# Optimization experiments

Measured on AMD Instinct MI355X. Metric: run time of the kernel, lower is better.

The kernel has to match this reference:

```python
import jax, jax.numpy as jnp
import numpy as np

B, N, K = 16, 4096, 128

def setup_inputs() -> dict:
    key = jax.random.key(0)
    k1, k2, k3, k4, k5 = jax.random.split(key, 5)
    positions = jax.random.normal(k1, (B, N, 3), dtype=jnp.float32) * 5.0
    neighbors = jax.random.randint(k2, (B, N, K), 0, N, dtype=jnp.int32)
    neighbor_mask = (jax.random.uniform(k3, (B, N, K)) < 0.9).astype(jnp.float32)
    cell = jax.random.normal(k4, (B, 3, 3), dtype=jnp.float32) + 10.0 * jnp.eye(3, dtype=jnp.float32)
    cell_offsets = jax.random.randint(k5, (B, N, K, 3), -1, 2).astype(jnp.float32)
    return {
        "positions": positions,
        "neighbors": neighbors,
        "neighbor_mask": neighbor_mask,
        "cell": cell,
        "cell_offsets": cell_offsets,
    }

def reference(positions, neighbors, neighbor_mask, cell, cell_offsets):
    # Gather neighbor positions: [B,N,K,3]
    pos_j = jax.vmap(lambda p, n: p[n])(positions, neighbors)
    # Relative vectors r_j - r_i
    dist_vec = pos_j - positions[:, :, None, :]
    # Periodic boundary correction: offsets @ cell, [B,N,K,3]
    dist_vec = dist_vec + jnp.einsum("bnkd,bde->bnke", cell_offsets, cell)
    sq = jnp.sum(dist_vec * dist_vec, axis=-1)  # [B,N,K]
    mask = neighbor_mask > 0
    # Masked distances (safe sqrt: avoid sqrt(0) grad issues on masked entries)
    distances = jnp.where(mask, jnp.sqrt(jnp.where(mask, sq, 1.0)), 0.0)
    return distances
```

## Files before the change

### kernel.cpp

```cpp
#include <hip/hip_runtime.h>
#include <math.h>

constexpr int B = 16;
constexpr int N = 4096;
constexpr int K = 128;

constexpr int ROWS_PER_BLOCK = 128;
constexpr int THREADS = 512;
constexpr int EPC     = THREADS * 4;
constexpr int CHUNKS  = (ROWS_PER_BLOCK * K) / EPC;
constexpr int SLOTS   = 4;
constexpr int AHEAD   = 3;

typedef float fx4 __attribute__((ext_vector_type(4)));
typedef int   ix4 __attribute__((ext_vector_type(4)));


struct Chunk {
    ix4 jj;
    fx4 mm, o0, o1, o2;
};

__device__ __forceinline__ void load_chunk(Chunk& c,
                                           const int*   __restrict__ nbr,
                                           const float* __restrict__ mask,
                                           const float* __restrict__ offs,
                                           size_t e0) {
    c.jj = __builtin_nontemporal_load((const ix4*)(nbr  + e0));
    c.mm = __builtin_nontemporal_load((const fx4*)(mask + e0));
    const fx4* __restrict__ p = (const fx4*)(offs + e0 * 3);
    c.o0 = p[0];
    c.o1 = p[1];
    c.o2 = p[2];
}

__global__ __launch_bounds__(THREADS, 4)
void pairwise_dist_deep(const float* __restrict__ pos,
                        const int*   __restrict__ nbr,
                        const float* __restrict__ mask,
                        const float* __restrict__ cell,
                        const float* __restrict__ offs,
                        float*       __restrict__ out) {
    __shared__ fx4 spos[N];

    const int tid   = threadIdx.x;
    const int b     = blockIdx.x >> 5;
    const int rblk  = blockIdx.x & 31;
    const int nbase = rblk * ROWS_PER_BLOCK;

    {
        const fx4* __restrict__ pb4 = (const fx4*)(pos + (size_t)b * N * 3);
        const fx4 r0 = pb4[tid * 6 + 0];
        const fx4 r1 = pb4[tid * 6 + 1];
        const fx4 r2 = pb4[tid * 6 + 2];
        const fx4 r3 = pb4[tid * 6 + 3];
        const fx4 r4 = pb4[tid * 6 + 4];
        const fx4 r5 = pb4[tid * 6 + 5];
        const int a0 = tid * 8;
        spos[a0 + 0] = (fx4){r0.x, r0.y, r0.z, 0.f};
        spos[a0 + 1] = (fx4){r0.w, r1.x, r1.y, 0.f};
        spos[a0 + 2] = (fx4){r1.z, r1.w, r2.x, 0.f};
        spos[a0 + 3] = (fx4){r2.y, r2.z, r2.w, 0.f};
        spos[a0 + 4] = (fx4){r3.x, r3.y, r3.z, 0.f};
        spos[a0 + 5] = (fx4){r3.w, r4.x, r4.y, 0.f};
        spos[a0 + 6] = (fx4){r4.z, r4.w, r5.x, 0.f};
        spos[a0 + 7] = (fx4){r5.y, r5.z, r5.w, 0.f};
    }

    const float* __restrict__ cb = cell + b * 9;
    const float c00 = cb[0], c01 = cb[1], c02 = cb[2];
    const float c10 = cb[3], c11 = cb[4], c12 = cb[5];
    const float c20 = cb[6], c21 = cb[7], c22 = cb[8];

    const size_t blockElemBase = ((size_t)b * N + nbase) * K;

    Chunk win[SLOTS];
#pragma unroll
    for (int c = 0; c < AHEAD; ++c)
        load_chunk(win[c], nbr, mask, offs,
                   blockElemBase + (size_t)c * EPC + (size_t)tid * 4);
    __builtin_amdgcn_sched_barrier(0);

    __syncthreads();

#pragma unroll
    for (int c = 0; c < CHUNKS; ++c) {
        if (c + AHEAD < CHUNKS) {
            load_chunk(win[(c + AHEAD) % SLOTS], nbr, mask, offs,
                       blockElemBase + (size_t)(c + AHEAD) * EPC +
                       (size_t)tid * 4);
            __builtin_amdgcn_sched_barrier(0);
        }

        const Chunk& cur = win[c % SLOTS];

        const int    eLocal = c * EPC + tid * 4;
        const size_t e0     = blockElemBase + eLocal;
        const int    n      = nbase + (eLocal >> 7);
        const fx4    pi     = spos[n];

        const float ox[4] = {cur.o0.x, cur.o0.w, cur.o1.z, cur.o2.y};
        const float oy[4] = {cur.o0.y, cur.o1.x, cur.o1.w, cur.o2.z};
        const float oz[4] = {cur.o0.z, cur.o1.y, cur.o2.x, cur.o2.w};
        const int   j [4] = {cur.jj.x, cur.jj.y, cur.jj.z, cur.jj.w};
        const float m [4] = {cur.mm.x, cur.mm.y, cur.mm.z, cur.mm.w};

        float res[4];
#pragma unroll
        for (int i = 0; i < 4; ++i) {
            const fx4 pj = spos[j[i]];
            const float dx = (pj.x - pi.x) + ox[i] * c00 + oy[i] * c10 + oz[i] * c20;
            const float dy = (pj.y - pi.y) + ox[i] * c01 + oy[i] * c11 + oz[i] * c21;
            const float dz = (pj.z - pi.z) + ox[i] * c02 + oy[i] * c12 + oz[i] * c22;
            const float sq = dx * dx + dy * dy + dz * dz;
            res[i] = (m[i] > 0.0f) ? __builtin_amdgcn_sqrtf(sq) : 0.0f;
        }

        const fx4 r = {res[0], res[1], res[2], res[3]};
        __builtin_nontemporal_store(r, (fx4*)(out + e0));
    }
}

extern "C" void kernel_launch(void* const* d_in, const int* in_sizes, int n_in,
                              void* d_out, int out_size, void* d_ws, size_t ws_size,
                              hipStream_t stream) {
    const float* positions     = (const float*)d_in[0];
    const int*   neighbors     = (const int*)  d_in[1];
    const float* neighbor_mask = (const float*)d_in[2];
    const float* cell          = (const float*)d_in[3];
    const float* cell_offsets  = (const float*)d_in[4];
    float*       out           = (float*)d_out;

    const int blocks = B * (N / ROWS_PER_BLOCK);

    pairwise_dist_deep<<<blocks, THREADS, 0, stream>>>(
        positions, neighbors, neighbor_mask, cell, cell_offsets, out);
}
```

Measured before the change: 209.2 us.

## Stage streamed inputs through LDS with direct global-to-LDS async loads

```diff
diff --git a/kernel.cpp b/kernel.cpp
--- a/kernel.cpp
+++ b/kernel.cpp
@@ -7,46 +7,121 @@
 
 constexpr int ROWS_PER_BLOCK = 128;
 constexpr int THREADS = 512;
+constexpr int WAVES   = THREADS / 64;
 constexpr int EPC     = THREADS * 4;
 constexpr int CHUNKS  = (ROWS_PER_BLOCK * K) / EPC;
-constexpr int SLOTS   = 4;
-constexpr int AHEAD   = 3;
+constexpr int DEPTH   = 2;
+
+constexpr int SLAB_B  = 5 * 1024;
+
 
 typedef float fx4 __attribute__((ext_vector_type(4)));
 typedef int   ix4 __attribute__((ext_vector_type(4)));
 
+#define AS1(p) ((const __attribute__((address_space(1))) void*)(p))
+#define AS3(p) ((__attribute__((address_space(3))) void*)(p))
 
-struct Chunk {
-    ix4 jj;
-    fx4 mm, o0, o1, o2;
+struct Ctx {
+    const int*   nbr;
+    const float* mask;
+    const float* offs;
+    float*       out;
+    size_t base;
+    int    nbase, wv, lane;
+    float  c00, c01, c02, c10, c11, c12, c20, c21, c22;
 };
 
-__device__ __forceinline__ void load_chunk(Chunk& c,
-                                           const int*   __restrict__ nbr,
-                                           const float* __restrict__ mask,
-                                           const float* __restrict__ offs,
-                                           size_t e0) {
-    c.jj = __builtin_nontemporal_load((const ix4*)(nbr  + e0));
-    c.mm = __builtin_nontemporal_load((const fx4*)(mask + e0));
-    const fx4* __restrict__ p = (const fx4*)(offs + e0 * 3);
-    c.o0 = p[0];
-    c.o1 = p[1];
-    c.o2 = p[2];
+template<int CC>
+__device__ __forceinline__ void stage_chunk(const Ctx& x, char* slabs) {
+    constexpr int slot = CC & (DEPTH - 1);
+    char* slab = slabs + slot * (WAVES * SLAB_B);
+    const size_t slice = x.base + (size_t)CC * EPC + (size_t)x.wv * 256;
+    const int*   gn = x.nbr  + slice     + x.lane * 4;
+    const float* gm = x.mask + slice     + x.lane * 4;
+    const float* go = x.offs + slice * 3 + x.lane * 4;
+    __builtin_amdgcn_global_load_lds(AS1(gn),       AS3(slab),        16, 0, 0);
+    __builtin_amdgcn_global_load_lds(AS1(gm),       AS3(slab + 1024), 16, 0, 0);
+    __builtin_amdgcn_global_load_lds(AS1(go),       AS3(slab + 2048), 16, 0, 0);
+    __builtin_amdgcn_global_load_lds(AS1(go + 256), AS3(slab + 3072), 16, 0, 0);
+    __builtin_amdgcn_global_load_lds(AS1(go + 512), AS3(slab + 4096), 16, 0, 0);
+    __builtin_amdgcn_sched_barrier(0);
 }
 
-__global__ __launch_bounds__(THREADS, 4)
-void pairwise_dist_deep(const float* __restrict__ pos,
-                        const int*   __restrict__ nbr,
-                        const float* __restrict__ mask,
-                        const float* __restrict__ cell,
-                        const float* __restrict__ offs,
-                        float*       __restrict__ out) {
+template<int C>
+__device__ __forceinline__ void chunk_body(const Ctx& x, const fx4* spos,
+                                           char* slabs) {
+    constexpr int slot = C & (DEPTH - 1);
+    constexpr int NW = (C == 0) ? 5 : ((C == CHUNKS - 1) ? 1 : 6);
+    asm volatile("s_waitcnt vmcnt(%0)" :: "n"(NW) : "memory");
+    __builtin_amdgcn_sched_barrier(0);
+
+    const char* slab = slabs + slot * (WAVES * SLAB_B);
+    const ix4 jj = *(const ix4*)(slab + x.lane * 16);
+    const fx4 mm = *(const fx4*)(slab + 1024 + x.lane * 16);
+    const char* ob = slab + 2048 + x.lane * 48;
+    const fx4 o0 = *(const fx4*)(ob);
+    const fx4 o1 = *(const fx4*)(ob + 16);
+    const fx4 o2 = *(const fx4*)(ob + 32);
+
+    const int n  = x.nbase + C * (EPC / K) + x.wv * 2 + (x.lane >> 5);
+    const fx4 pi = spos[n];
+
+    const float ox[4] = {o0.x, o0.w, o1.z, o2.y};
+    const float oy[4] = {o0.y, o1.x, o1.w, o2.z};
+    const float oz[4] = {o0.z, o1.y, o2.x, o2.w};
+    const int   j [4] = {jj.x, jj.y, jj.z, jj.w};
+    const float m [4] = {mm.x, mm.y, mm.z, mm.w};
+
+    float res[4];
+#pragma unroll
+    for (int i = 0; i < 4; ++i) {
+        const fx4 pj = spos[j[i]];
+        const float dx = (pj.x - pi.x) + ox[i]*x.c00 + oy[i]*x.c10 + oz[i]*x.c20;
+        const float dy = (pj.y - pi.y) + ox[i]*x.c01 + oy[i]*x.c11 + oz[i]*x.c21;
+        const float dz = (pj.z - pi.z) + ox[i]*x.c02 + oy[i]*x.c12 + oz[i]*x.c22;
+        const float sq = dx*dx + dy*dy + dz*dz;
+        res[i] = (m[i] > 0.0f) ? __builtin_amdgcn_sqrtf(sq) : 0.0f;
+    }
+    const fx4 r = {res[0], res[1], res[2], res[3]};
+    const size_t e0 = x.base + (size_t)C * EPC + (size_t)x.wv * 256
+                      + (size_t)x.lane * 4;
+    __builtin_nontemporal_store(r, (fx4*)(x.out + e0));
+
+    if constexpr (C + DEPTH < CHUNKS) {
+        asm volatile("s_waitcnt lgkmcnt(0)" ::: "memory");
+        __builtin_amdgcn_sched_barrier(0);
+        stage_chunk<C + DEPTH>(x, slabs);
+    }
+}
+
+template<int C>
+__device__ __forceinline__ void run_chunks(const Ctx& x, const fx4* spos,
+                                           char* slabs) {
+    chunk_body<C>(x, spos, slabs);
+    if constexpr (C + 1 < CHUNKS) run_chunks<C + 1>(x, spos, slabs);
+}
+
+__global__ __launch_bounds__(THREADS)
+void pairwise_dist_dma(const float* __restrict__ pos,
+                       const int*   __restrict__ nbr,
+                       const float* __restrict__ mask,
+                       const float* __restrict__ cell,
+                       const float* __restrict__ offs,
+                       float*       __restrict__ out) {
     __shared__ fx4 spos[N];
+    __shared__ fx4 stagebuf[DEPTH][WAVES][SLAB_B / 16];
 
     const int tid   = threadIdx.x;
+    const int wv    = tid >> 6;
+    const int lane  = tid & 63;
     const int b     = blockIdx.x >> 5;
     const int rblk  = blockIdx.x & 31;
     const int nbase = rblk * ROWS_PER_BLOCK;
+
+    const float* __restrict__ cb = cell + b * 9;
+    const float c00 = cb[0], c01 = cb[1], c02 = cb[2];
+    const float c10 = cb[3], c11 = cb[4], c12 = cb[5];
+    const float c20 = cb[6], c21 = cb[7], c22 = cb[8];
 
     {
         const fx4* __restrict__ pb4 = (const fx4*)(pos + (size_t)b * N * 3);
@@ -67,58 +142,24 @@
         spos[a0 + 7] = (fx4){r5.y, r5.z, r5.w, 0.f};
     }
 
-    const float* __restrict__ cb = cell + b * 9;
-    const float c00 = cb[0], c01 = cb[1], c02 = cb[2];
-    const float c10 = cb[3], c11 = cb[4], c12 = cb[5];
-    const float c20 = cb[6], c21 = cb[7], c22 = cb[8];
+    Ctx x;
+    x.nbr = nbr; x.mask = mask; x.offs = offs; x.out = out;
+    x.base  = ((size_t)b * N + nbase) * K;
+    x.nbase = nbase; x.wv = wv; x.lane = lane;
+    x.c00 = c00; x.c01 = c01; x.c02 = c02;
+    x.c10 = c10; x.c11 = c11; x.c12 = c12;
+    x.c20 = c20; x.c21 = c21; x.c22 = c22;
 
-    const size_t blockElemBase = ((size_t)b * N + nbase) * K;
+    char* slabs = (char*)&stagebuf[0][wv][0];
 
-    Chunk win[SLOTS];
-#pragma unroll
-    for (int c = 0; c < AHEAD; ++c)
-        load_chunk(win[c], nbr, mask, offs,
-                   blockElemBase + (size_t)c * EPC + (size_t)tid * 4);
+    stage_chunk<0>(x, slabs);
+    stage_chunk<1>(x, slabs);
+
+    asm volatile("s_waitcnt lgkmcnt(0)" ::: "memory");
+    __builtin_amdgcn_s_barrier();
     __builtin_amdgcn_sched_barrier(0);
 
-    __syncthreads();
-
-#pragma unroll
-    for (int c = 0; c < CHUNKS; ++c) {
-        if (c + AHEAD < CHUNKS) {
-            load_chunk(win[(c + AHEAD) % SLOTS], nbr, mask, offs,
-                       blockElemBase + (size_t)(c + AHEAD) * EPC +
-                       (size_t)tid * 4);
-            __builtin_amdgcn_sched_barrier(0);
-        }
-
-        const Chunk& cur = win[c % SLOTS];
-
-        const int    eLocal = c * EPC + tid * 4;
-        const size_t e0     = blockElemBase + eLocal;
-        const int    n      = nbase + (eLocal >> 7);
-        const fx4    pi     = spos[n];
-
-        const float ox[4] = {cur.o0.x, cur.o0.w, cur.o1.z, cur.o2.y};
-        const float oy[4] = {cur.o0.y, cur.o1.x, cur.o1.w, cur.o2.z};
-        const float oz[4] = {cur.o0.z, cur.o1.y, cur.o2.x, cur.o2.w};
-        const int   j [4] = {cur.jj.x, cur.jj.y, cur.jj.z, cur.jj.w};
-        const float m [4] = {cur.mm.x, cur.mm.y, cur.mm.z, cur.mm.w};
-
-        float res[4];
-#pragma unroll
-        for (int i = 0; i < 4; ++i) {
-            const fx4 pj = spos[j[i]];
-            const float dx = (pj.x - pi.x) + ox[i] * c00 + oy[i] * c10 + oz[i] * c20;
-            const float dy = (pj.y - pi.y) + ox[i] * c01 + oy[i] * c11 + oz[i] * c21;
-            const float dz = (pj.z - pi.z) + ox[i] * c02 + oy[i] * c12 + oz[i] * c22;
-            const float sq = dx * dx + dy * dy + dz * dz;
-            res[i] = (m[i] > 0.0f) ? __builtin_amdgcn_sqrtf(sq) : 0.0f;
-        }
-
-        const fx4 r = {res[0], res[1], res[2], res[3]};
-        __builtin_nontemporal_store(r, (fx4*)(out + e0));
-    }
+    run_chunks<0>(x, spos, slabs);
 }
 
 extern "C" void kernel_launch(void* const* d_in, const int* in_sizes, int n_in,
@@ -133,6 +174,6 @@
 
     const int blocks = B * (N / ROWS_PER_BLOCK);
 
-    pairwise_dist_deep<<<blocks, THREADS, 0, stream>>>(
+    pairwise_dist_dma<<<blocks, THREADS, 0, stream>>>(
         positions, neighbors, neighbor_mask, cell, cell_offsets, out);
 }
```

Measured after the change: 212.8 us. No clear change (+1.7%).
